# Performance work log

Hardware: AMD Instinct MI355X
Metric: run time of the kernel (lower is better)

Reference implementation:

```python
import jax, jax.numpy as jnp
import numpy as np

B, N, M, K = 128, 128, 16, 8      # graphs, nodes/graph, num_samples, pearl_k
H_MLP = 16                        # pearl_mlp_out
D_PE = 64                         # pe_dims (GIN hidden/out)
E = 262144
BN_EPS = 1e-5


def setup_inputs() -> dict:
    key = jax.random.key(0)
    ks = jax.random.split(key, 16)
    lap = jax.random.normal(ks[0], (B, N, N), dtype=jnp.float32) * 0.1
    W0 = jax.random.normal(ks[1], (B, N, M), dtype=jnp.float32)
    edge_index = jax.random.randint(ks[2], (2, E), 0, B * N, dtype=jnp.int32)
    s = lambda k, sh, fan: jax.random.normal(k, sh, dtype=jnp.float32) / np.sqrt(fan)
    return {
        "lap": lap,
        "W0": W0,
        "mlp_W": s(ks[3], (K, H_MLP), K),
        "mlp_b": jnp.zeros((H_MLP,), jnp.float32),
        "bn_g": jnp.ones((H_MLP,), jnp.float32),
        "bn_b": jnp.zeros((H_MLP,), jnp.float32),
        "eps1": jnp.zeros((), jnp.float32),
        "W1a": s(ks[4], (H_MLP, D_PE), H_MLP),
        "b1a": jnp.zeros((D_PE,), jnp.float32),
        "W1b": s(ks[5], (D_PE, D_PE), D_PE),
        "b1b": jnp.zeros((D_PE,), jnp.float32),
        "eps2": jnp.zeros((), jnp.float32),
        "W2a": s(ks[6], (D_PE, D_PE), D_PE),
        "b2a": jnp.zeros((D_PE,), jnp.float32),
        "W2b": s(ks[7], (D_PE, D_PE), D_PE),
        "b2b": jnp.zeros((D_PE,), jnp.float32),
        "edge_index": edge_index,
    }


def _gin_layer(h, eps, Wa, ba, Wb, bb, src, dst, num_nodes):
    # h: [Nsum, M, D]; GIN aggregation: (1+eps)*h + sum_{j in N(i)} h_j
    agg = jax.ops.segment_sum(h[src], dst, num_segments=num_nodes)
    z = (1.0 + eps) * h + agg
    z = jax.nn.relu(jnp.einsum("nmd,de->nme", z, Wa) + ba)
    z = jnp.einsum("nmd,de->nme", z, Wb) + bb
    return jax.nn.relu(z)


def reference(lap, W0, mlp_W, mlp_b, bn_g, bn_b, eps1, W1a, b1a, W1b, b1b,
              eps2, W2a, b2a, W2b, b2b, edge_index):
    # polynomial filter: stack [W, S@W, S^2@W, ...]  -> [B, N, M, K]
    out = W0
    ws = [out]
    for _ in range(K - 1):
        out = jnp.einsum("bij,bjm->bim", lap, out)
        ws.append(out)
    feat = jnp.stack(ws, axis=-1)                       # [B, N, M, K]

    # per-graph MLP over trailing k dim + BatchNorm1d (training stats, per graph)
    h = jnp.einsum("bnmk,kh->bnmh", feat, mlp_W) + mlp_b  # [B, N, M, H]
    mu = jnp.mean(h, axis=(1, 2), keepdims=True)
    var = jnp.var(h, axis=(1, 2), keepdims=True)
    h = (h - mu) * jax.lax.rsqrt(var + BN_EPS) * bn_g + bn_b
    h = jax.nn.relu(h)

    # concat graphs -> [Nsum, M, H]; GIN over batched edge_index
    h = h.reshape(B * N, M, H_MLP)
    src, dst = edge_index[0], edge_index[1]
    h = _gin_layer(h, eps1, W1a, b1a, W1b, b1b, src, dst, B * N)
    h = _gin_layer(h, eps2, W2a, b2a, W2b, b2b, src, dst, B * N)

    # RandomSampleAggregator: sum over the sample dim -> [Nsum, D_pe]
    return h.sum(axis=1)
```

## Files before the change

### kernel.cpp

```cpp
#include <hip/hip_runtime.h>

typedef unsigned short u16;
typedef unsigned int   u32;
typedef short bf16x8 __attribute__((ext_vector_type(8)));
typedef float f32x4  __attribute__((ext_vector_type(4)));
typedef float f32x2  __attribute__((ext_vector_type(2)));

#define BG    128
#define NN    128
#define MS    16
#define KP    8
#define HM    16
#define DP    64
#define NSUM  16384
#define NE    262144
#define SITES 2048


__device__ __forceinline__ float blo(u32 u){ union{u32 i; float f;} v; v.i=u<<16; return v.f; }
__device__ __forceinline__ float bhi(u32 u){ union{u32 i; float f;} v; v.i=u&0xffff0000u; return v.f; }
__device__ __forceinline__ u16  f2b(float f){ union{float f; u32 i;} v; v.f=f; u32 x=v.i; x += 0x7fffu + ((x>>16)&1u); return (u16)(x>>16); }
__device__ __forceinline__ u32  pk2(float a, float b){ return (u32)f2b(a) | ((u32)f2b(b)<<16); }
__device__ __forceinline__ f32x2 up2(u32 u){ f32x2 v; v.x=blo(u); v.y=bhi(u); return v; }

__device__ __forceinline__ void fsplit(float x, short& hi, short& lo){
  u16 h = f2b(x); hi = (short)h; lo = (short)f2b(x - blo((u32)h));
}

__device__ __forceinline__ void acc4s(float* a, uint2 x, float s){
  a[0]+=s*blo(x.x); a[1]+=s*bhi(x.x); a[2]+=s*blo(x.y); a[3]+=s*bhi(x.y);
}

#define MFMA16(a,b,c) __builtin_amdgcn_mfma_f32_16x16x32_bf16(a,b,c,0,0,0)

__device__ __forceinline__ bf16x8 bfragW(const float* __restrict__ W, int nrows,
                                         int k0, int nb, int col, int quad){
  bf16x8 f;
  #pragma unroll
  for(int j=0;j<8;++j){
    int k = k0 + quad*8 + j;
    float v = (k < nrows) ? W[k*DP + nb + col] : 0.f;
    f[j] = (short)f2b(v);
  }
  return f;
}
__device__ __forceinline__ bf16x8 afragT(const float* tp){
  float4 v0 = *(const float4*)tp;
  float4 v1 = *(const float4*)(tp+4);
  bf16x8 a;
  a[0]=(short)f2b(v0.x); a[1]=(short)f2b(v0.y); a[2]=(short)f2b(v0.z); a[3]=(short)f2b(v0.w);
  a[4]=(short)f2b(v1.x); a[5]=(short)f2b(v1.y); a[6]=(short)f2b(v1.z); a[7]=(short)f2b(v1.w);
  return a;
}

__global__ __launch_bounds__(256,1) void k_poly(
    const float* __restrict__ lap, const float* __restrict__ W0, const float* __restrict__ mlpW,
    const float* __restrict__ bng, const float* __restrict__ bnb, u16* __restrict__ h1,
    int* __restrict__ cnt)
{
  __shared__ float Wbuf[2][SITES];
  __shared__ float mlpWS[KP*HM];
  __shared__ float red[4][32];
  __shared__ float stat[32];
  __shared__ float ssc[HM], ssh[HM];

  const int b = blockIdx.x, t = threadIdx.x, l = t&63, w = t>>6;
  const int col = l&15, quad = l>>4;
  if (t < 128) cnt[b*128 + t] = 0;

  {
    const float4* src = (const float4*)(W0 + (size_t)b*SITES);
    for (int i=t; i<SITES/4; i+=256) ((float4*)Wbuf[0])[i] = src[i];
    if (t < KP*HM) mlpWS[t] = mlpW[t];
  }

  bf16x8 Ah[2][4], Al[2][4];
  {
    const float* lg = lap + (size_t)b*NN*NN;
    #pragma unroll
    for(int Mt=0;Mt<2;++Mt){
      const int nr = w*32 + Mt*16 + col;
      #pragma unroll
      for(int Kc=0;Kc<4;++Kc){
        const float* p = lg + (size_t)nr*NN + Kc*32 + quad*8;
        float4 v0 = *(const float4*)p;
        float4 v1 = *(const float4*)(p+4);
        float xs[8] = {v0.x,v0.y,v0.z,v0.w,v1.x,v1.y,v1.z,v1.w};
        #pragma unroll
        for(int j=0;j<8;++j){ short hi,lo; fsplit(xs[j],hi,lo); Ah[Mt][Kc][j]=hi; Al[Mt][Kc][j]=lo; }
      }
    }
  }

  float h[8][16];
  {
    const float* w0g = W0 + (size_t)b*SITES;
    #pragma unroll
    for(int Mt=0;Mt<2;++Mt){
      #pragma unroll
      for(int r=0;r<4;++r){
        const int n = w*32 + Mt*16 + quad*4 + r;
        float sv = w0g[n*MS + col];
        #pragma unroll
        for(int c=0;c<16;++c) h[Mt*4+r][c] = sv*mlpW[c];
      }
    }
  }
  __syncthreads();

  int cur=0;
  for(int k=1;k<KP;++k){
    f32x4 c0 = {0.f,0.f,0.f,0.f};
    f32x4 c1 = {0.f,0.f,0.f,0.f};
    #pragma unroll
    for(int Kc=0;Kc<4;++Kc){
      const float* wb = &Wbuf[cur][(Kc*32 + quad*8)*MS + col];
      bf16x8 Bh, Bl;
      #pragma unroll
      for(int j=0;j<8;++j){
        float x = wb[j*MS];
        short hi,lo; fsplit(x,hi,lo); Bh[j]=hi; Bl[j]=lo;
      }
      c0 = MFMA16(Ah[0][Kc], Bh, c0);
      c0 = MFMA16(Ah[0][Kc], Bl, c0);
      c0 = MFMA16(Al[0][Kc], Bh, c0);
      c1 = MFMA16(Ah[1][Kc], Bh, c1);
      c1 = MFMA16(Ah[1][Kc], Bl, c1);
      c1 = MFMA16(Al[1][Kc], Bh, c1);
    }
    float mw[16];
    #pragma unroll
    for(int c=0;c<16;++c) mw[c]=mlpWS[k*16+c];
    #pragma unroll
    for(int r=0;r<4;++r){
      const int n0 = w*32 + quad*4 + r;
      Wbuf[cur^1][n0*MS + col]        = c0[r];
      Wbuf[cur^1][(n0+16)*MS + col]   = c1[r];
      #pragma unroll
      for(int c=0;c<16;++c){ h[r][c] += c0[r]*mw[c]; h[4+r][c] += c1[r]*mw[c]; }
    }
    __syncthreads();
    cur ^= 1;
  }

  float sum[16], sq[16];
  #pragma unroll
  for(int c=0;c<16;++c){ sum[c]=0.f; sq[c]=0.f; }
  #pragma unroll
  for(int s=0;s<8;++s){
    #pragma unroll
    for(int c=0;c<16;++c){ float v=h[s][c]; sum[c]+=v; sq[c]+=v*v; }
  }
  #pragma unroll
  for(int d=1;d<64;d<<=1){
    #pragma unroll
    for(int c=0;c<16;++c){ sum[c]+=__shfl_xor(sum[c],d,64); sq[c]+=__shfl_xor(sq[c],d,64); }
  }
  if(l==0){
    #pragma unroll
    for(int c=0;c<16;++c){ red[w][c]=sum[c]; red[w][16+c]=sq[c]; }
  }
  __syncthreads();
  if(t<32) stat[t]=red[0][t]+red[1][t]+red[2][t]+red[3][t];
  __syncthreads();
  if(t<16){
    float mu  = stat[t]*(1.f/SITES);
    float var = stat[16+t]*(1.f/SITES) - mu*mu;
    float sc  = bng[t] * rsqrtf(var + 1e-5f);
    ssc[t]=sc; ssh[t]=bnb[t] - mu*sc;
  }
  __syncthreads();
  {
    float sc[16], sh[16];
    #pragma unroll
    for(int c=0;c<16;++c){ sc[c]=ssc[c]; sh[c]=ssh[c]; }
    #pragma unroll
    for(int s=0;s<8;++s){
      const int n = w*32 + (s>>2)*16 + quad*4 + (s&3);
      const int node = b*NN + n;
      float r[16];
      #pragma unroll
      for(int c=0;c<16;++c) r[c]=fmaxf(h[s][c]*sc[c]+sh[c], 0.f);
      uint4 A;
      A.x=pk2(r[0],r[1]);  A.y=pk2(r[2],r[3]);  A.z=pk2(r[4],r[5]);  A.w=pk2(r[6],r[7]);
      uint4 Bv;
      Bv.x=pk2(r[8],r[9]); Bv.y=pk2(r[10],r[11]); Bv.z=pk2(r[12],r[13]); Bv.w=pk2(r[14],r[15]);
      u16* o = h1 + (size_t)node*256 + (size_t)col*HM;
      *(uint4*)o     = A;
      *(uint4*)(o+8) = Bv;
    }
  }
}

__global__ void k_hist(const int* __restrict__ dst, int* __restrict__ cnt){
  int e = blockIdx.x*256 + threadIdx.x;
  atomicAdd(&cnt[dst[e]], 1);
}

__global__ void k_scan(const int* __restrict__ cnt, int* __restrict__ off, int* __restrict__ wpos){
  __shared__ int ps[256];
  const int t = threadIdx.x, PER = NSUM/256;
  int s=0;
  for(int i=0;i<PER;++i) s += cnt[t*PER+i];
  ps[t]=s; __syncthreads();
  for(int d=1; d<256; d<<=1){
    int v = (t>=d) ? ps[t-d] : 0;
    __syncthreads();
    ps[t] += v;
    __syncthreads();
  }
  int run = (t==0) ? 0 : ps[t-1];
  for(int i=0;i<PER;++i){
    int idx=t*PER+i;
    off[idx]=run; wpos[idx]=run;
    run += cnt[idx];
  }
  if(t==255) off[NSUM]=run;
}

__global__ void k_scatter(const int* __restrict__ srcI, const int* __restrict__ dstI,
                          int* __restrict__ wpos, int* __restrict__ srcs){
  int e = blockIdx.x*256 + threadIdx.x;
  int p = atomicAdd(&wpos[dstI[e]], 1);
  srcs[p] = srcI[e];
}

__global__ __launch_bounds__(256) void k_agg1(
  const u16* __restrict__ h1, const float* __restrict__ eps1p,
  const int* __restrict__ off, const int* __restrict__ srcs, u16* __restrict__ z1)
{
  const int t=threadIdx.x, l=t&63;
  const int node = blockIdx.x*4 + (t>>6);
  const float epe = 1.f + eps1p[0];
  float a[4] = {0.f,0.f,0.f,0.f};
  acc4s(a, *(const uint2*)&h1[(size_t)node*256 + l*4], epe);
  int e=off[node]; const int e1=off[node+1];
  for(; e+8<=e1; e+=8){
    int s0=srcs[e],s1=srcs[e+1],s2=srcs[e+2],s3=srcs[e+3];
    int s4=srcs[e+4],s5=srcs[e+5],s6=srcs[e+6],s7=srcs[e+7];
    uint2 r0=*(const uint2*)&h1[(size_t)s0*256 + l*4];
    uint2 r1=*(const uint2*)&h1[(size_t)s1*256 + l*4];
    uint2 r2=*(const uint2*)&h1[(size_t)s2*256 + l*4];
    uint2 r3=*(const uint2*)&h1[(size_t)s3*256 + l*4];
    uint2 r4=*(const uint2*)&h1[(size_t)s4*256 + l*4];
    uint2 r5=*(const uint2*)&h1[(size_t)s5*256 + l*4];
    uint2 r6=*(const uint2*)&h1[(size_t)s6*256 + l*4];
    uint2 r7=*(const uint2*)&h1[(size_t)s7*256 + l*4];
    acc4s(a,r0,1.f); acc4s(a,r1,1.f); acc4s(a,r2,1.f); acc4s(a,r3,1.f);
    acc4s(a,r4,1.f); acc4s(a,r5,1.f); acc4s(a,r6,1.f); acc4s(a,r7,1.f);
  }
  for(; e<e1; ++e){
    uint2 r=*(const uint2*)&h1[(size_t)srcs[e]*256 + l*4];
    acc4s(a,r,1.f);
  }
  uint2 o; o.x=pk2(a[0],a[1]); o.y=pk2(a[2],a[3]);
  *(uint2*)&z1[(size_t)node*256 + l*4] = o;
}

__global__ __launch_bounds__(256) void k_agg2(
  const u16* __restrict__ h2T, const float* __restrict__ eps2p,
  const int* __restrict__ off, const int* __restrict__ srcs, u16* __restrict__ z2)
{
  const int t=threadIdx.x, l=t&63, w=t>>6;
  const int m = blockIdx.x & 15, g = blockIdx.x >> 4;
  const int grp = l>>3, q = l&7;
  const int node = g*32 + w*8 + grp;
  const float epe = 1.f + eps2p[0];
  const u16* __restrict__ base = h2T + (size_t)m*NSUM*DP;

  f32x2 A[4];
  {
    uint4 x = *(const uint4*)&base[(size_t)node*DP + q*8];
    f32x2 s2; s2.x=epe; s2.y=epe;
    A[0]=s2*up2(x.x); A[1]=s2*up2(x.y); A[2]=s2*up2(x.z); A[3]=s2*up2(x.w);
  }
  const int e0 = off[node], e1 = off[node+1];
  int dmax = e1 - e0;
  #pragma unroll
  for(int d=1; d<64; d<<=1) dmax = max(dmax, __shfl_xor(dmax, d, 64));

  int i = 0;
  for(; i+2 <= dmax; i += 2){
    int pa = e0+i, pb = e0+i+1;
    float sa = (pa < e1) ? 1.f : 0.f;
    float sb = (pb < e1) ? 1.f : 0.f;
    int ea = min(pa, NE-1), eb = min(pb, NE-1);
    int ia = srcs[ea], ib = srcs[eb];
    uint4 xa = *(const uint4*)&base[(size_t)ia*DP + q*8];
    uint4 xb = *(const uint4*)&base[(size_t)ib*DP + q*8];
    f32x2 va; va.x=sa; va.y=sa;
    f32x2 vb; vb.x=sb; vb.y=sb;
    A[0]+=va*up2(xa.x); A[1]+=va*up2(xa.y); A[2]+=va*up2(xa.z); A[3]+=va*up2(xa.w);
    A[0]+=vb*up2(xb.x); A[1]+=vb*up2(xb.y); A[2]+=vb*up2(xb.z); A[3]+=vb*up2(xb.w);
  }
  if(i < dmax){
    int pa = e0+i;
    float sa = (pa < e1) ? 1.f : 0.f;
    int ea = min(pa, NE-1);
    int ia = srcs[ea];
    uint4 xa = *(const uint4*)&base[(size_t)ia*DP + q*8];
    f32x2 va; va.x=sa; va.y=sa;
    A[0]+=va*up2(xa.x); A[1]+=va*up2(xa.y); A[2]+=va*up2(xa.z); A[3]+=va*up2(xa.w);
  }

  uint4 o;
  o.x=pk2(A[0].x,A[0].y); o.y=pk2(A[1].x,A[1].y);
  o.z=pk2(A[2].x,A[2].y); o.w=pk2(A[3].x,A[3].y);
  *(uint4*)&z2[(size_t)node*1024 + m*DP + q*8] = o;
}

__global__ __launch_bounds__(256) void k_mm1(
  const u16* __restrict__ z1, const float* __restrict__ W1a, const float* __restrict__ b1a,
  const float* __restrict__ W1b, const float* __restrict__ b1b, u16* __restrict__ h2T)
{
  __shared__ float tS[4][16*68 + 4];
  const int t=threadIdx.x, l=t&63, w=t>>6;
  const int col=l&15, quad=l>>4;

  bf16x8 fa[4], fb[4][2];
  float bav[4], bbv[4];
  #pragma unroll
  for(int nt=0;nt<4;++nt){
    fa[nt]    = bfragW(W1a, HM, 0,  nt*16, col, quad);
    fb[nt][0] = bfragW(W1b, DP, 0,  nt*16, col, quad);
    fb[nt][1] = bfragW(W1b, DP, 32, nt*16, col, quad);
    bav[nt] = b1a[nt*16+col];
    bbv[nt] = b1b[nt*16+col];
  }
  for(int ni=0;ni<2;++ni){
    const int node = blockIdx.x*8 + ni*4 + w;
    bf16x8 a0;
    #pragma unroll
    for(int j=0;j<8;++j) a0[j]=0;
    if (quad < 2) a0 = *(const bf16x8*)&z1[(size_t)node*256 + col*16 + quad*8];
    #pragma unroll
    for(int nt=0;nt<4;++nt){
      f32x4 c = {bav[nt], bav[nt], bav[nt], bav[nt]};
      c = MFMA16(a0, fa[nt], c);
      #pragma unroll
      for(int r=0;r<4;++r)
        tS[w][(quad*4+r)*68 + nt*16 + col] = fmaxf(c[r], 0.f);
    }
    bf16x8 ta0 = afragT(&tS[w][col*68 + quad*8]);
    bf16x8 ta1 = afragT(&tS[w][col*68 + 32 + quad*8]);
    #pragma unroll
    for(int nt=0;nt<4;++nt){
      f32x4 c = {bbv[nt], bbv[nt], bbv[nt], bbv[nt]};
      c = MFMA16(ta0, fb[nt][0], c);
      c = MFMA16(ta1, fb[nt][1], c);
      #pragma unroll
      for(int r=0;r<4;++r)
        h2T[((size_t)(quad*4+r)*NSUM + node)*DP + nt*16 + col] = f2b(fmaxf(c[r], 0.f));
    }
  }
}

__global__ __launch_bounds__(256) void k_mm2(
  const u16* __restrict__ z2, const float* __restrict__ W2a, const float* __restrict__ b2a,
  const float* __restrict__ W2b, const float* __restrict__ b2b, float* __restrict__ out)
{
  __shared__ float tS[4][16*68 + 4];
  const int t=threadIdx.x, l=t&63, w=t>>6;
  const int col=l&15, quad=l>>4;

  bf16x8 fa[4][2], fb[4][2];
  float bav[4], bbv[4];
  #pragma unroll
  for(int nt=0;nt<4;++nt){
    fa[nt][0] = bfragW(W2a, DP, 0,  nt*16, col, quad);
    fa[nt][1] = bfragW(W2a, DP, 32, nt*16, col, quad);
    fb[nt][0] = bfragW(W2b, DP, 0,  nt*16, col, quad);
    fb[nt][1] = bfragW(W2b, DP, 32, nt*16, col, quad);
    bav[nt] = b2a[nt*16+col];
    bbv[nt] = b2b[nt*16+col];
  }
  for(int ni=0;ni<2;++ni){
    const int node = blockIdx.x*8 + ni*4 + w;
    const u16* zrow = &z2[(size_t)node*1024];
    bf16x8 a0 = *(const bf16x8*)&zrow[col*64 + quad*8];
    bf16x8 a1 = *(const bf16x8*)&zrow[col*64 + quad*8 + 32];
    #pragma unroll
    for(int nt=0;nt<4;++nt){
      f32x4 c = {bav[nt], bav[nt], bav[nt], bav[nt]};
      c = MFMA16(a0, fa[nt][0], c);
      c = MFMA16(a1, fa[nt][1], c);
      #pragma unroll
      for(int r=0;r<4;++r)
        tS[w][(quad*4+r)*68 + nt*16 + col] = fmaxf(c[r], 0.f);
    }
    bf16x8 ta0 = afragT(&tS[w][col*68 + quad*8]);
    bf16x8 ta1 = afragT(&tS[w][col*68 + 32 + quad*8]);
    #pragma unroll
    for(int nt=0;nt<4;++nt){
      f32x4 c = {bbv[nt], bbv[nt], bbv[nt], bbv[nt]};
      c = MFMA16(ta0, fb[nt][0], c);
      c = MFMA16(ta1, fb[nt][1], c);
      float s = fmaxf(c[0],0.f)+fmaxf(c[1],0.f)+fmaxf(c[2],0.f)+fmaxf(c[3],0.f);
      s += __shfl_xor(s, 16, 64);
      s += __shfl_xor(s, 32, 64);
      if (quad == 0)
        out[(size_t)node*64 + nt*16 + col] = s;
    }
  }
}

extern "C" void kernel_launch(void* const* d_in, const int* in_sizes, int n_in,
                              void* d_out, int out_size, void* d_ws, size_t ws_size,
                              hipStream_t stream)
{
  (void)in_sizes; (void)n_in; (void)out_size; (void)ws_size;
  const float* lap  = (const float*)d_in[0];
  const float* W0   = (const float*)d_in[1];
  const float* mlpW = (const float*)d_in[2];
  const float* bng  = (const float*)d_in[4];
  const float* bnb  = (const float*)d_in[5];
  const float* eps1 = (const float*)d_in[6];
  const float* W1a  = (const float*)d_in[7];
  const float* b1a  = (const float*)d_in[8];
  const float* W1b  = (const float*)d_in[9];
  const float* b1b  = (const float*)d_in[10];
  const float* eps2 = (const float*)d_in[11];
  const float* W2a  = (const float*)d_in[12];
  const float* b2a  = (const float*)d_in[13];
  const float* W2b  = (const float*)d_in[14];
  const float* b2b  = (const float*)d_in[15];
  const int*   ei   = (const int*)d_in[16];
  const int* srcI = ei;
  const int* dstI = ei + NE;

  char* ws = (char*)d_ws;
  u16* h1   = (u16*)(ws);
  u16* z1   = (u16*)(ws + 8388608);
  u16* h2T  = (u16*)(ws + 16777216);
  u16* z2   = (u16*)(ws + 50331648);
  int* cnt  = (int*)(ws + 83886080);
  int* offA = (int*)(ws + 83951616);
  int* wpos = (int*)(ws + 84017408);
  int* srcs = (int*)(ws + 84082944);

  k_poly   <<<BG,      256, 0, stream>>>(lap, W0, mlpW, bng, bnb, h1, cnt);
  k_hist   <<<NE/256,  256, 0, stream>>>(dstI, cnt);
  k_scan   <<<1,       256, 0, stream>>>(cnt, offA, wpos);
  k_scatter<<<NE/256,  256, 0, stream>>>(srcI, dstI, wpos, srcs);
  k_agg1   <<<NSUM/4,  256, 0, stream>>>(h1, eps1, offA, srcs, z1);
  k_mm1    <<<NSUM/8,  256, 0, stream>>>(z1, W1a, b1a, W1b, b1b, h2T);
  k_agg2   <<<16*(NSUM/32), 256, 0, stream>>>(h2T, eps2, offA, srcs, z2);
  k_mm2    <<<NSUM/8,  256, 0, stream>>>(z2, W2a, b2a, W2b, b2b, (float*)d_out);
}
```

Measured before the change: 257.4 us.

## Store layer-1 features sample-major and aggregate per sample slice in agg1

k_poly now writes h1 transposed so that each sample m has a contiguous [node][16] slab, and k_agg1 launches one block per (sample, 64-node group) instead of one wave per node over all samples. Four lanes cover one node's 16 channels, and each wave walks neighbors in lockstep up to the wave-wide maximum degree, zeroing contributions that fall past a node's own edge range. The aim is a smaller, more cache-resident gather working set per sample slice. The cost is more index loads, since each edge's source is fetched once per sample, plus wasted iterations on degree imbalance and scattered 8-byte output writes.

```diff
diff --git a/kernel.cpp b/kernel.cpp
--- a/kernel.cpp
+++ b/kernel.cpp
@@ -27,10 +27,6 @@
   u16 h = f2b(x); hi = (short)h; lo = (short)f2b(x - blo((u32)h));
 }
 
-__device__ __forceinline__ void acc4s(float* a, uint2 x, float s){
-  a[0]+=s*blo(x.x); a[1]+=s*bhi(x.x); a[2]+=s*blo(x.y); a[3]+=s*bhi(x.y);
-}
-
 #define MFMA16(a,b,c) __builtin_amdgcn_mfma_f32_16x16x32_bf16(a,b,c,0,0,0)
 
 __device__ __forceinline__ bf16x8 bfragW(const float* __restrict__ W, int nrows,
@@ -55,7 +51,7 @@
 
 __global__ __launch_bounds__(256,1) void k_poly(
     const float* __restrict__ lap, const float* __restrict__ W0, const float* __restrict__ mlpW,
-    const float* __restrict__ bng, const float* __restrict__ bnb, u16* __restrict__ h1,
+    const float* __restrict__ bng, const float* __restrict__ bnb, u16* __restrict__ h1T,
     int* __restrict__ cnt)
 {
   __shared__ float Wbuf[2][SITES];
@@ -185,7 +181,7 @@
       A.x=pk2(r[0],r[1]);  A.y=pk2(r[2],r[3]);  A.z=pk2(r[4],r[5]);  A.w=pk2(r[6],r[7]);
       uint4 Bv;
       Bv.x=pk2(r[8],r[9]); Bv.y=pk2(r[10],r[11]); Bv.z=pk2(r[12],r[13]); Bv.w=pk2(r[14],r[15]);
-      u16* o = h1 + (size_t)node*256 + (size_t)col*HM;
+      u16* o = h1T + ((size_t)col*NSUM + node)*HM;
       *(uint4*)o     = A;
       *(uint4*)(o+8) = Bv;
     }
@@ -226,35 +222,53 @@
 }
 
 __global__ __launch_bounds__(256) void k_agg1(
-  const u16* __restrict__ h1, const float* __restrict__ eps1p,
+  const u16* __restrict__ h1T, const float* __restrict__ eps1p,
   const int* __restrict__ off, const int* __restrict__ srcs, u16* __restrict__ z1)
 {
-  const int t=threadIdx.x, l=t&63;
-  const int node = blockIdx.x*4 + (t>>6);
+  const int t=threadIdx.x, l=t&63, w=t>>6;
+  const int m = blockIdx.x & 15, g = blockIdx.x >> 4;
+  const int grp = l>>2, q = l&3;
+  const int node = g*64 + w*16 + grp;
   const float epe = 1.f + eps1p[0];
-  float a[4] = {0.f,0.f,0.f,0.f};
-  acc4s(a, *(const uint2*)&h1[(size_t)node*256 + l*4], epe);
-  int e=off[node]; const int e1=off[node+1];
-  for(; e+8<=e1; e+=8){
-    int s0=srcs[e],s1=srcs[e+1],s2=srcs[e+2],s3=srcs[e+3];
-    int s4=srcs[e+4],s5=srcs[e+5],s6=srcs[e+6],s7=srcs[e+7];
-    uint2 r0=*(const uint2*)&h1[(size_t)s0*256 + l*4];
-    uint2 r1=*(const uint2*)&h1[(size_t)s1*256 + l*4];
-    uint2 r2=*(const uint2*)&h1[(size_t)s2*256 + l*4];
-    uint2 r3=*(const uint2*)&h1[(size_t)s3*256 + l*4];
-    uint2 r4=*(const uint2*)&h1[(size_t)s4*256 + l*4];
-    uint2 r5=*(const uint2*)&h1[(size_t)s5*256 + l*4];
-    uint2 r6=*(const uint2*)&h1[(size_t)s6*256 + l*4];
-    uint2 r7=*(const uint2*)&h1[(size_t)s7*256 + l*4];
-    acc4s(a,r0,1.f); acc4s(a,r1,1.f); acc4s(a,r2,1.f); acc4s(a,r3,1.f);
-    acc4s(a,r4,1.f); acc4s(a,r5,1.f); acc4s(a,r6,1.f); acc4s(a,r7,1.f);
-  }
-  for(; e<e1; ++e){
-    uint2 r=*(const uint2*)&h1[(size_t)srcs[e]*256 + l*4];
-    acc4s(a,r,1.f);
-  }
-  uint2 o; o.x=pk2(a[0],a[1]); o.y=pk2(a[2],a[3]);
-  *(uint2*)&z1[(size_t)node*256 + l*4] = o;
+  const u16* __restrict__ base = h1T + (size_t)m*NSUM*HM;
+
+  f32x2 A[2];
+  {
+    uint2 x = *(const uint2*)&base[(size_t)node*HM + q*4];
+    f32x2 s2; s2.x=epe; s2.y=epe;
+    A[0]=s2*up2(x.x); A[1]=s2*up2(x.y);
+  }
+  const int e0 = off[node], e1 = off[node+1];
+  int dmax = e1 - e0;
+  #pragma unroll
+  for(int d=1; d<64; d<<=1) dmax = max(dmax, __shfl_xor(dmax, d, 64));
+
+  int i = 0;
+  for(; i+2 <= dmax; i += 2){
+    int pa = e0+i, pb = e0+i+1;
+    float sa = (pa < e1) ? 1.f : 0.f;
+    float sb = (pb < e1) ? 1.f : 0.f;
+    int ea = min(pa, NE-1), eb = min(pb, NE-1);
+    int ia = srcs[ea], ib = srcs[eb];
+    uint2 xa = *(const uint2*)&base[(size_t)ia*HM + q*4];
+    uint2 xb = *(const uint2*)&base[(size_t)ib*HM + q*4];
+    f32x2 va; va.x=sa; va.y=sa;
+    f32x2 vb; vb.x=sb; vb.y=sb;
+    A[0]+=va*up2(xa.x); A[1]+=va*up2(xa.y);
+    A[0]+=vb*up2(xb.x); A[1]+=vb*up2(xb.y);
+  }
+  if(i < dmax){
+    int pa = e0+i;
+    float sa = (pa < e1) ? 1.f : 0.f;
+    int ea = min(pa, NE-1);
+    int ia = srcs[ea];
+    uint2 xa = *(const uint2*)&base[(size_t)ia*HM + q*4];
+    f32x2 va; va.x=sa; va.y=sa;
+    A[0]+=va*up2(xa.x); A[1]+=va*up2(xa.y);
+  }
+
+  uint2 o; o.x=pk2(A[0].x,A[0].y); o.y=pk2(A[1].x,A[1].y);
+  *(uint2*)&z1[(size_t)node*256 + m*HM + q*4] = o;
 }
 
 __global__ __launch_bounds__(256) void k_agg2(
@@ -429,7 +443,7 @@
   const int* dstI = ei + NE;
 
   char* ws = (char*)d_ws;
-  u16* h1   = (u16*)(ws);
+  u16* h1T  = (u16*)(ws);
   u16* z1   = (u16*)(ws + 8388608);
   u16* h2T  = (u16*)(ws + 16777216);
   u16* z2   = (u16*)(ws + 50331648);
@@ -438,11 +452,11 @@
   int* wpos = (int*)(ws + 84017408);
   int* srcs = (int*)(ws + 84082944);
 
-  k_poly   <<<BG,      256, 0, stream>>>(lap, W0, mlpW, bng, bnb, h1, cnt);
+  k_poly   <<<BG,      256, 0, stream>>>(lap, W0, mlpW, bng, bnb, h1T, cnt);
   k_hist   <<<NE/256,  256, 0, stream>>>(dstI, cnt);
   k_scan   <<<1,       256, 0, stream>>>(cnt, offA, wpos);
   k_scatter<<<NE/256,  256, 0, stream>>>(srcI, dstI, wpos, srcs);
-  k_agg1   <<<NSUM/4,  256, 0, stream>>>(h1, eps1, offA, srcs, z1);
+  k_agg1   <<<16*(NSUM/64), 256, 0, stream>>>(h1T, eps1, offA, srcs, z1);
   k_mm1    <<<NSUM/8,  256, 0, stream>>>(z1, W1a, b1a, W1b, b1b, h2T);
   k_agg2   <<<16*(NSUM/32), 256, 0, stream>>>(h2T, eps2, offA, srcs, z2);
   k_mm2    <<<NSUM/8,  256, 0, stream>>>(z2, W2a, b2a, W2b, b2b, (float*)d_out);
```

Measured after the change: 274.7 us. 6.7% more time.
